# Performance work log

Measured on AMD Instinct MI355X. Metric: run time of the kernel, lower is better.

Reference implementation:

```python
import jax, jax.numpy as jnp
import numpy as np

D = 1024       # d_model
H = 16         # n_heads
N = 8          # ortho_dim
NSKEW = N * (N - 1) // 2
MAX_ANGLE = 0.5
B, T = 4, 4096
IDX_I, IDX_J = np.triu_indices(N, k=1)


def setup_inputs() -> dict:
    key = jax.random.key(0)
    ks = jax.random.split(key, 8)
    s = 0.02
    w = lambda k, shape: jax.random.normal(k, shape, jnp.float32) * s
    return {
        "x": jax.random.normal(ks[0], (B, T, D), jnp.float32),
        "W_skew": w(ks[1], (D, H * NSKEW)),
        "W_k": w(ks[2], (D, H * N)),
        "W_v": w(ks[3], (D, H * N)),
        "W_q": w(ks[4], (D, H * N)),
        "W_beta": w(ks[5], (D, H)),
        "b_beta": w(ks[6], (H,)),
        "W_o": w(ks[7], (H * N, D)),
    }


def _forward(x, W_skew, W_k, W_v, W_q, W_beta, b_beta, W_o):
    Bb, Tt, _ = x.shape
    # skew-symmetric generator -> rotation O_t = expm(skew)
    skew_flat = MAX_ANGLE * jnp.tanh(x @ W_skew).reshape(Bb, Tt, H, NSKEW)
    skew = jnp.zeros((Bb, Tt, H, N, N), x.dtype)
    skew = skew.at[..., IDX_I, IDX_J].set(skew_flat)
    skew = skew.at[..., IDX_J, IDX_I].set(-skew_flat)
    O = jax.vmap(jax.scipy.linalg.expm)(skew.reshape(-1, N, N)).reshape(Bb, Tt, H, N, N)

    k = (x @ W_k).reshape(Bb, Tt, H, N)
    k = k / jnp.maximum(jnp.linalg.norm(k, axis=-1, keepdims=True), 1e-6)
    v = (x @ W_v).reshape(Bb, Tt, H, N)
    q = (x @ W_q).reshape(Bb, Tt, H, N)
    beta = jax.nn.sigmoid(x @ W_beta + b_beta)  # [B,T,H]

    def step(c, inp):
        O_t, k_t, v_t, b_t, q_t = inp  # [B,H,n,n], [B,H,n], ...
        # rotation conjugation: O c O^T
        c_rot = jnp.einsum('bhij,bhjk,bhlk->bhil', O_t, c, O_t)
        # rank-1 erase: c_rot - beta * k (k^T c_rot); rank-1 write: + beta * k v^T
        kc = jnp.einsum('bhi,bhij->bhj', k_t, c_rot)
        b = b_t[..., None, None]
        c_new = c_rot - b * k_t[..., None] * kc[..., None, :] + b * k_t[..., None] * v_t[..., None, :]
        o_t = jnp.einsum('bhi,bhij->bhj', q_t, c_new)  # readout q . c_t
        return c_new, o_t

    c0 = jnp.zeros((Bb, H, N, N), x.dtype)
    tfirst = lambda a: jnp.moveaxis(a, 1, 0)
    _, o = jax.lax.scan(step, c0, (tfirst(O), tfirst(k), tfirst(v), tfirst(beta), tfirst(q)))
    o = jnp.moveaxis(o, 0, 1).reshape(Bb, Tt, H * N)
    return o @ W_o


def reference(x, W_skew, W_k, W_v, W_q, W_beta, b_beta, W_o):
    return _forward(x, W_skew, W_k, W_v, W_q, W_beta, b_beta, W_o)
```

## Files before the change

### kernel.cpp

```cpp
#include <hip/hip_runtime.h>

typedef unsigned short u16;
typedef unsigned int u32;
typedef __attribute__((ext_vector_type(4))) float f32x4;
typedef __attribute__((ext_vector_type(8))) short short8;
typedef __attribute__((ext_vector_type(4))) unsigned int u32x4;

#define DEV __device__ __forceinline__

DEV float bf2f(u16 u){ union{u32 i; float f;} x; x.i = ((u32)u)<<16; return x.f; }
DEV u16 f2bf(float f){ union{u32 i; float f;} x; x.f = f; u32 r = x.i + 0x7fffu + ((x.i>>16)&1u); return (u16)(r>>16); }

union U8 { u16 u[8]; short8 s; };

DEV void gl16(const u16* g, u16* l){
  __builtin_amdgcn_global_load_lds(
      (const __attribute__((address_space(1))) u32*)g,
      (__attribute__((address_space(3))) u32*)l, 16, 0, 0);
}

DEV float fast_htanh(float v){
  float vc = fminf(fmaxf(v, -15.f), 15.f);
  float e = __expf(2.f*vc);
  return 0.5f*(e - 1.f)*__builtin_amdgcn_rcpf(e + 1.f);
}
DEV float fast_sigmoid(float v){
  float e = __expf(-v);
  return __builtin_amdgcn_rcpf(1.f + e);
}

__global__ __launch_bounds__(256) void concat_kernel(
    const float* __restrict__ Wskew, const float* __restrict__ Wk, const float* __restrict__ Wv,
    const float* __restrict__ Wq, const float* __restrict__ Wbeta, const float* __restrict__ Wo,
    u16* __restrict__ Wh, u16* __restrict__ Wl, u16* __restrict__ WoT)
{
  int idx = blockIdx.x*256 + threadIdx.x;
  if (idx < 896*1024){
    int n = idx >> 10, kk = idx & 1023;
    float v;
    if (n < 448)      v = Wskew[kk*448 + n];
    else if (n < 576) v = Wk[kk*128 + (n-448)];
    else if (n < 704) v = Wv[kk*128 + (n-576)];
    else if (n < 832) v = Wq[kk*128 + (n-704)];
    else if (n < 848) v = Wbeta[kk*16 + (n-832)];
    else              v = 0.f;
    u16 h = f2bf(v);
    Wh[idx] = h;
    Wl[idx] = f2bf(v - bf2f(h));
  } else {
    int r = idx - 896*1024;
    int n = r >> 7, kk = r & 127;
    WoT[r] = f2bf(Wo[kk*1024 + n]);
  }
}

__global__ __launch_bounds__(256) void gemm_proj_kernel(
    const float* __restrict__ X,
    const u16* __restrict__ Bh, const u16* __restrict__ Bl,
    float* __restrict__ C, const float* __restrict__ bias)
{
  __shared__ u16 L[2*4*4096];
  const int tid = threadIdx.x;
  const int wave = tid >> 6;
  const int lane = tid & 63;
  const int quad = lane >> 4, l15 = lane & 15;
  const int m0 = blockIdx.x * 128, n0 = blockIdx.y * 128;
  const bool full = (blockIdx.y < 4);
  const int wm = (wave >> 1) * 64, wn = (wave & 1) * 64;
  const bool wantLow = full && !(blockIdx.y == 3 && wn == 64);
  const bool skipBl1 = (blockIdx.y == 3);
  const int K = 1024, ldc = 896;
  const int sr = tid >> 2;
  const int sc = tid & 3;
  const int fS = (sr & 3) ^ ((sr >> 2) & 3);
  const int scS = ((sc ^ fS) << 3);
  const size_t gA0 = (size_t)(m0 + sr)*K + scS, gA1 = gA0 + (size_t)64*K;
  const size_t gB0 = (size_t)(n0 + sr)*K + scS, gB1 = gB0 + (size_t)64*K;
  const int d0 = tid*8, d1 = d0 + 2048;
  const int fR = (l15 & 3) ^ ((l15 >> 2) & 3);
  const int rq = ((quad ^ fR) << 3);

  auto LOADA = [&](int kb, f32x4* va){
    va[0] = *(const f32x4*)(X + gA0 + kb);
    va[1] = *(const f32x4*)(X + gA0 + kb + 4);
    va[2] = *(const f32x4*)(X + gA1 + kb);
    va[3] = *(const f32x4*)(X + gA1 + kb + 4);
  };
  auto WRITEA = [&](int buf, const f32x4* va){
    u16* Lb = L + buf*16384;
    U8 h0, h1;
    #pragma unroll
    for (int e=0;e<4;e++){
      h0.u[e]   = f2bf(va[0][e]);
      h0.u[4+e] = f2bf(va[1][e]);
      h1.u[e]   = f2bf(va[2][e]);
      h1.u[4+e] = f2bf(va[3][e]);
    }
    *(short8*)&Lb[d0] = h0.s; *(short8*)&Lb[d1] = h1.s;
    if (full){
      U8 l0, l1;
      #pragma unroll
      for (int e=0;e<4;e++){
        l0.u[e]   = f2bf(va[0][e] - bf2f(h0.u[e]));
        l0.u[4+e] = f2bf(va[1][e] - bf2f(h0.u[4+e]));
        l1.u[e]   = f2bf(va[2][e] - bf2f(h1.u[e]));
        l1.u[4+e] = f2bf(va[3][e] - bf2f(h1.u[4+e]));
      }
      *(short8*)&Lb[8192+d0] = l0.s; *(short8*)&Lb[8192+d1] = l1.s;
    }
  };
  auto STAGEB = [&](int buf, int kb){
    u16* Lb = L + buf*16384;
    gl16(Bh + gB0 + kb, Lb + 4096 + d0);
    gl16(Bh + gB1 + kb, Lb + 4096 + d1);
    if (full){
      gl16(Bl + gB0 + kb, Lb + 12288 + d0);
      if (!skipBl1) gl16(Bl + gB1 + kb, Lb + 12288 + d1);
    }
  };

  f32x4 acc[4][4] = {};
  { f32x4 va[4]; LOADA(0, va); STAGEB(0, 0); WRITEA(0, va); }
  __syncthreads();
  int cur = 0;
  for (int kb = 0; kb < K; kb += 32){
    const bool hasNext = (kb + 32 < K);
    f32x4 vn[4];
    if (hasNext){ LOADA(kb + 32, vn); STAGEB(cur^1, kb + 32); }
    u16* Lb = L + cur*16384;
    short8 afh[4], bfh[4];
    #pragma unroll
    for (int mi=0;mi<4;mi++) afh[mi] = *(const short8*)&Lb[(wm + mi*16 + l15)*32 + rq];
    #pragma unroll
    for (int ni=0;ni<4;ni++) bfh[ni] = *(const short8*)&Lb[4096 + (wn + ni*16 + l15)*32 + rq];
    #pragma unroll
    for (int mi=0;mi<4;mi++)
      #pragma unroll
      for (int ni=0;ni<4;ni++)
        acc[mi][ni] = __builtin_amdgcn_mfma_f32_16x16x32_bf16(afh[mi], bfh[ni], acc[mi][ni], 0,0,0);
    if (wantLow){
      short8 afl[4], bfl[4];
      #pragma unroll
      for (int mi=0;mi<4;mi++) afl[mi] = *(const short8*)&Lb[8192 + (wm + mi*16 + l15)*32 + rq];
      #pragma unroll
      for (int ni=0;ni<4;ni++) bfl[ni] = *(const short8*)&Lb[12288 + (wn + ni*16 + l15)*32 + rq];
      #pragma unroll
      for (int mi=0;mi<4;mi++)
        #pragma unroll
        for (int ni=0;ni<4;ni++){
          acc[mi][ni] = __builtin_amdgcn_mfma_f32_16x16x32_bf16(afh[mi], bfl[ni], acc[mi][ni], 0,0,0);
          acc[mi][ni] = __builtin_amdgcn_mfma_f32_16x16x32_bf16(afl[mi], bfh[ni], acc[mi][ni], 0,0,0);
        }
    }
    if (hasNext) WRITEA(cur^1, vn);
    __syncthreads();
    cur ^= 1;
  }
  #pragma unroll
  for (int mi=0;mi<4;mi++){
    #pragma unroll
    for (int ni=0;ni<4;ni++){
      const int col = n0 + wn + ni*16 + l15;
      const int rb_ = m0 + wm + mi*16 + quad*4;
      #pragma unroll
      for (int r=0;r<4;r++){
        float v = acc[mi][ni][r];
        const int row = rb_ + r;
        if (col < 448) v = fast_htanh(v);
        else if (col >= 832 && col < 848) v = fast_sigmoid(v + bias[col-832]);
        C[(size_t)row*ldc + col] = v;
      }
    }
  }
}

__global__ __launch_bounds__(256) void gemm_out_kernel(
    const u16* __restrict__ A, const u16* __restrict__ Bt, float* __restrict__ C)
{
  __shared__ u16 L[2*2*4096];
  const int tid = threadIdx.x;
  const int wave = tid >> 6;
  const int lane = tid & 63;
  const int quad = lane >> 4, l15 = lane & 15;
  const int m0 = blockIdx.x * 128, n0 = blockIdx.y * 128;
  const int wm = (wave >> 1) * 64, wn = (wave & 1) * 64;
  const int K = 128, ldc = 1024;
  const int sr = tid >> 2;
  const int sc = tid & 3;
  const int fS = (sr & 3) ^ ((sr >> 2) & 3);
  const int scS = ((sc ^ fS) << 3);
  const size_t gA0 = (size_t)(m0 + sr)*K + scS, gA1 = gA0 + (size_t)64*K;
  const size_t gB0 = (size_t)(n0 + sr)*K + scS, gB1 = gB0 + (size_t)64*K;
  const int d0 = tid*8, d1 = d0 + 2048;
  const int fR = (l15 & 3) ^ ((l15 >> 2) & 3);
  const int rq = ((quad ^ fR) << 3);

  auto STAGE = [&](int buf, int kb){
    u16* Lb = L + buf*8192;
    gl16(A  + gA0 + kb, Lb + d0);
    gl16(A  + gA1 + kb, Lb + d1);
    gl16(Bt + gB0 + kb, Lb + 4096 + d0);
    gl16(Bt + gB1 + kb, Lb + 4096 + d1);
  };

  f32x4 acc[4][4] = {};
  STAGE(0, 0);
  __syncthreads();
  int cur = 0;
  for (int kb = 0; kb < K; kb += 32){
    if (kb + 32 < K) STAGE(cur^1, kb + 32);
    u16* Lb = L + cur*8192;
    short8 af[4], bf8[4];
    #pragma unroll
    for (int mi=0;mi<4;mi++) af[mi] = *(const short8*)&Lb[(wm + mi*16 + l15)*32 + rq];
    #pragma unroll
    for (int ni=0;ni<4;ni++) bf8[ni] = *(const short8*)&Lb[4096 + (wn + ni*16 + l15)*32 + rq];
    #pragma unroll
    for (int mi=0;mi<4;mi++)
      #pragma unroll
      for (int ni=0;ni<4;ni++)
        acc[mi][ni] = __builtin_amdgcn_mfma_f32_16x16x32_bf16(af[mi], bf8[ni], acc[mi][ni], 0,0,0);
    __syncthreads();
    cur ^= 1;
  }
  #pragma unroll
  for (int mi=0;mi<4;mi++)
    #pragma unroll
    for (int ni=0;ni<4;ni++){
      const int col = n0 + wn + ni*16 + l15;
      const int rb_ = m0 + wm + mi*16 + quad*4;
      #pragma unroll
      for (int r=0;r<4;r++)
        C[(size_t)(rb_ + r)*ldc + col] = acc[mi][ni][r];
    }
}

__device__ constexpr int TRI_I[28] = {0,0,0,0,0,0,0, 1,1,1,1,1,1, 2,2,2,2,2, 3,3,3,3, 4,4,4, 5,5, 6};
__device__ constexpr int TRI_J[28] = {1,2,3,4,5,6,7, 2,3,4,5,6,7, 3,4,5,6,7, 4,5,6,7, 5,6,7, 6,7, 7};

__global__ __launch_bounds__(64, 1) void expm_scan_kernel(const float* __restrict__ proj, float* __restrict__ OR)
{
  __shared__ float S0[16*64*4];
  const int t = threadIdx.x;
  const int s = blockIdx.x >> 6, c = blockIdx.x & 63;
  const int b = s >> 4, h = s & 15;
  const int row = b*4096 + c*64 + t;
  const float* sk = proj + (size_t)row*896 + h*28;

  float v[28];
  {
    f32x4 vv[7];
    #pragma unroll
    for (int i=0;i<7;i++) vv[i] = *(const f32x4*)(sk + 4*i);
    #pragma unroll
    for (int i=0;i<28;i++) v[i] = vv[i>>2][i&3] * 0.0625f;
  }

  float M[64], T[64];
  auto bmul = [&](const float* Min, float* Tout){
    #pragma unroll
    for (int i=0;i<8;i++){
      #pragma unroll
      for (int cc=0;cc<8;cc++){
        float acc = 0.f;
        #pragma unroll
        for (int a=0;a<8;a++){
          if (a == i) continue;
          const int k = (i<a) ? (i*7 - (i*(i-1))/2 + a - i - 1)
                              : (a*7 - (a*(a-1))/2 + i - a - 1);
          if (i<a) acc = fmaf( v[k], Min[a*8+cc], acc);
          else     acc = fmaf(-v[k], Min[a*8+cc], acc);
        }
        Tout[i*8+cc] = acc;
      }
    }
  };
  #pragma unroll
  for (int i=0;i<8;i++){
    #pragma unroll
    for (int jj=0;jj<8;jj++){
      float bv = 0.f;
      if (i < jj){ const int k = i*7 - (i*(i-1))/2 + jj - i - 1; bv =  v[k]; }
      if (i > jj){ const int k = jj*7 - (jj*(jj-1))/2 + i - jj - 1; bv = -v[k]; }
      M[i*8+jj] = bv*(1.f/6.f) + ((i==jj)?1.f:0.f);
    }
  }
  const float coef[5] = {0.2f, 0.25f, 1.f/3.f, 0.5f, 1.f};
  #pragma unroll
  for (int st=0; st<5; st++){
    bmul(M, T);
    #pragma unroll
    for (int i=0;i<8;i++)
      #pragma unroll
      for (int jj=0;jj<8;jj++)
        M[i*8+jj] = T[i*8+jj]*coef[st] + ((i==jj)?1.f:0.f);
  }
  #pragma unroll
  for (int sq=0; sq<4; sq++){
    #pragma unroll
    for (int i=0;i<8;i++)
      #pragma unroll
      for (int cc=0;cc<8;cc++){
        float acc = 0.f;
        #pragma unroll
        for (int a=0;a<8;a++) acc = fmaf(M[i*8+a], M[a*8+cc], acc);
        T[i*8+cc] = acc;
      }
    #pragma unroll
    for (int f=0;f<64;f++) M[f] = T[f];
  }
  #pragma unroll
  for (int j=0;j<16;j++){
    f32x4 w = {M[4*j], M[4*j+1], M[4*j+2], M[4*j+3]};
    *(f32x4*)&S0[(j*64 + t)*4] = w;
  }
  __syncthreads();

  #pragma unroll
  for (int d=0; d<6; d++){
    const int off = 1 << d;
    if (t >= off){
      float Q[64];
      #pragma unroll
      for (int j=0;j<16;j++){
        f32x4 x = *(const f32x4*)&S0[(j*64 + (t-off))*4];
        Q[4*j]=x[0]; Q[4*j+1]=x[1]; Q[4*j+2]=x[2]; Q[4*j+3]=x[3];
      }
      #pragma unroll
      for (int i=0;i<8;i++){
        float r[8];
        #pragma unroll
        for (int cc=0;cc<8;cc++){
          float acc = 0.f;
          #pragma unroll
          for (int a=0;a<8;a++) acc = fmaf(M[i*8+a], Q[a*8+cc], acc);
          r[cc] = acc;
        }
        #pragma unroll
        for (int cc=0;cc<8;cc++) M[i*8+cc] = r[cc];
      }
    }
    if (d < 5){
      #pragma unroll
      for (int j=0;j<16;j++){
        f32x4 w = {M[4*j], M[4*j+1], M[4*j+2], M[4*j+3]};
        *(f32x4*)&S0[(j*64 + t)*4] = w;
      }
      __syncthreads();
    }
  }

  float* dst = OR + ((size_t)s*4096 + (size_t)c*64 + t)*64;
  #pragma unroll
  for (int j=0;j<16;j++){
    const int rb = 4*(j&1), col = j>>1;
    f32x4 w = {M[(rb+0)*8 + col], M[(rb+1)*8 + col], M[(rb+2)*8 + col], M[(rb+3)*8 + col]};
    *(f32x4*)(dst + 4*j) = w;
  }
}

DEV void load16(const float* p, f32x4* M){
  #pragma unroll
  for (int q=0;q<16;q++) M[q] = *(const f32x4*)(p + 4*q);
}
DEV void rm_matvec8(const f32x4* M16, const float* x, float* res){
  #pragma unroll
  for (int i=0;i<8;i++){
    float acc = 0.f;
    #pragma unroll
    for (int a=0;a<8;a++) acc = fmaf(M16[2*i + (a>>2)][a&3], x[a], acc);
    res[i] = acc;
  }
}
DEV void cm_matvec8(const f32x4* M16, const float* x, float* res){
  #pragma unroll
  for (int i=0;i<8;i++){
    float acc = 0.f;
    #pragma unroll
    for (int a=0;a<8;a++) acc = fmaf(M16[2*a + (i>>2)][i&3], x[a], acc);
    res[i] = acc;
  }
}

__global__ __launch_bounds__(64, 1) void chunkscan_kernel(const float* __restrict__ OR, float* __restrict__ Rbase)
{
  __shared__ float S[64*68];
  const int t = threadIdx.x;
  const int s = blockIdx.x;
  float M[64];
  const float* qs = OR + ((size_t)s*4096 + (size_t)t*64 + 63)*64;
  #pragma unroll
  for (int j=0;j<16;j++){
    f32x4 x = *(const f32x4*)(qs + 4*j);
    M[4*j]=x[0]; M[4*j+1]=x[1]; M[4*j+2]=x[2]; M[4*j+3]=x[3];
  }
  #pragma unroll
  for (int j=0;j<16;j++){
    f32x4 w = {M[4*j],M[4*j+1],M[4*j+2],M[4*j+3]};
    *(f32x4*)&S[t*68 + 4*j] = w;
  }
  __syncthreads();
  #pragma unroll
  for (int d=0; d<6; d++){
    const int off = 1 << d;
    if (t >= off){
      float Q[64];
      const float* p = &S[(t-off)*68];
      #pragma unroll
      for (int j=0;j<16;j++){
        f32x4 x = *(const f32x4*)(p + 4*j);
        Q[4*j]=x[0]; Q[4*j+1]=x[1]; Q[4*j+2]=x[2]; Q[4*j+3]=x[3];
      }
      float R[64];
      #pragma unroll
      for (int cc=0;cc<8;cc++)
        #pragma unroll
        for (int i=0;i<8;i++){
          float acc = 0.f;
          #pragma unroll
          for (int a=0;a<8;a++) acc = fmaf(M[a*8+i], Q[cc*8+a], acc);
          R[cc*8+i] = acc;
        }
      #pragma unroll
      for (int f=0;f<64;f++) M[f] = R[f];
    }
    if (d < 5){
      #pragma unroll
      for (int j=0;j<16;j++){
        f32x4 w = {M[4*j],M[4*j+1],M[4*j+2],M[4*j+3]};
        *(f32x4*)&S[t*68 + 4*j] = w;
      }
      __syncthreads();
    }
  }
  if (t < 63){
    float* dst = Rbase + ((size_t)s*64 + t + 1)*64;
    #pragma unroll
    for (int j=0;j<16;j++){
      f32x4 w = {M[4*j],M[4*j+1],M[4*j+2],M[4*j+3]};
      *(f32x4*)(dst + 4*j) = w;
    }
  }
  if (t == 0){
    float* dst = Rbase + (size_t)s*64*64;
    #pragma unroll
    for (int cc=0;cc<8;cc++)
      #pragma unroll
      for (int i=0;i<8;i++) dst[cc*8+i] = (i==cc) ? 1.f : 0.f;
  }
}

__global__ __launch_bounds__(256) void rotate_kvq_kernel(const float* __restrict__ OR, const float* __restrict__ Rbase,
    float* __restrict__ proj)
{
  int tid = blockIdx.x*256 + threadIdx.x;
  int s = tid >> 12, t = tid & 4095;
  int c = t >> 6;
  int b = s >> 4, h = s & 15;
  int row = b*4096 + t;
  const float* slot = OR + ((size_t)s*4096 + t)*64;
  float* pr = proj + (size_t)row*896;
  float k[8], v[8], q[8];
  { f32x4 a = *(const f32x4*)(pr+448+h*8), b2 = *(const f32x4*)(pr+452+h*8);
    #pragma unroll
    for (int i=0;i<4;i++){ k[i]=a[i]; k[4+i]=b2[i]; } }
  { f32x4 a = *(const f32x4*)(pr+576+h*8), b2 = *(const f32x4*)(pr+580+h*8);
    #pragma unroll
    for (int i=0;i<4;i++){ v[i]=a[i]; v[4+i]=b2[i]; } }
  { f32x4 a = *(const f32x4*)(pr+704+h*8), b2 = *(const f32x4*)(pr+708+h*8);
    #pragma unroll
    for (int i=0;i<4;i++){ q[i]=a[i]; q[4+i]=b2[i]; } }
  float nn = 0.f;
  #pragma unroll
  for (int i=0;i<8;i++) nn = fmaf(k[i],k[i],nn);
  float inv = 1.f / fmaxf(sqrtf(nn), 1e-6f);
  #pragma unroll
  for (int i=0;i<8;i++) k[i] *= inv;

  f32x4 M[16];
  load16(slot, M);
  float uk[8], uv[8], uq[8];
  rm_matvec8(M, k, uk);
  rm_matvec8(M, v, uv);
  rm_matvec8(M, q, uq);
  load16(Rbase + ((size_t)s*64 + c)*64, M);
  float kt[8], vt[8], qt[8];
  rm_matvec8(M, uk, kt);
  rm_matvec8(M, uv, vt);
  rm_matvec8(M, uq, qt);

  float beta = pr[832+h];
  float qk = 0.f;
  #pragma unroll
  for (int j=0;j<8;j++) qk = fmaf(kt[j], qt[j], qk);
  float* sip = pr + h*28;
  f32x4 w0={kt[0],kt[1],kt[2],kt[3]}, w1={kt[4],kt[5],kt[6],kt[7]};
  f32x4 w2={vt[0],vt[1],vt[2],vt[3]}, w3={vt[4],vt[5],vt[6],vt[7]};
  f32x4 w4={qt[0],qt[1],qt[2],qt[3]}, w5={qt[4],qt[5],qt[6],qt[7]};
  f32x4 w6={beta, qk, 0.f, 0.f};
  *(f32x4*)(sip)=w0; *(f32x4*)(sip+4)=w1; *(f32x4*)(sip+8)=w2; *(f32x4*)(sip+12)=w3;
  *(f32x4*)(sip+16)=w4; *(f32x4*)(sip+20)=w5; *(f32x4*)(sip+24)=w6;
}

__global__ __launch_bounds__(256) void scan_pass1_kernel(const float* __restrict__ proj,
    float* __restrict__ Mbuf, float* __restrict__ wbuf)
{
  int tid = blockIdx.x*256 + threadIdx.x;
  int task = tid >> 3, j = tid & 7;
  int s = task >> 8, c = task & 255;
  int b = s >> 4, h = s & 15;
  const float* rec = proj + ((size_t)b*4096 + (size_t)c*16)*896 + h*28;
  float m[8], w[8];
  #pragma unroll
  for (int i=0;i<8;i++){ m[i] = (i==j)?1.f:0.f; w[i] = 0.f; }
  f32x4 k0 = *(const f32x4*)(rec), k1 = *(const f32x4*)(rec+4);
  float vt = rec[8+j];
  float beta = rec[24];
  for (int tt=0; tt<16; tt++){
    const float* pn = rec + (size_t)(tt+1)*896;
    f32x4 nk0 = *(const f32x4*)(pn), nk1 = *(const f32x4*)(pn+4);
    float nvt = pn[8+j];
    float nbeta = pn[24];
    float s1, s2;
    s1 = ((k0[0]*m[0] + k0[1]*m[1]) + (k0[2]*m[2] + k0[3]*m[3]))
       + ((k1[0]*m[4] + k1[1]*m[5]) + (k1[2]*m[6] + k1[3]*m[7]));
    s2 = ((k0[0]*w[0] + k0[1]*w[1]) + (k0[2]*w[2] + k0[3]*w[3]))
       + ((k1[0]*w[4] + k1[1]*w[5]) + (k1[2]*w[6] + k1[3]*w[7]));
    float c1 = -beta*s1, c2 = beta*(vt - s2);
    #pragma unroll
    for (int i=0;i<4;i++){ m[i] = fmaf(k0[i], c1, m[i]); m[4+i] = fmaf(k1[i], c1, m[4+i]); }
    #pragma unroll
    for (int i=0;i<4;i++){ w[i] = fmaf(k0[i], c2, w[i]); w[4+i] = fmaf(k1[i], c2, w[4+i]); }
    k0=nk0; k1=nk1; vt=nvt; beta=nbeta;
  }
  float* md = Mbuf + (size_t)task*64 + j*8;
  float* wd = wbuf + (size_t)task*64 + j*8;
  f32x4 m0={m[0],m[1],m[2],m[3]}, m1={m[4],m[5],m[6],m[7]};
  f32x4 w0={w[0],w[1],w[2],w[3]}, w1={w[4],w[5],w[6],w[7]};
  *(f32x4*)(md) = m0; *(f32x4*)(md+4) = m1;
  *(f32x4*)(wd) = w0; *(f32x4*)(wd+4) = w1;
}

__global__ __launch_bounds__(512) void scan_mid_kernel(const float* __restrict__ Mbuf,
    const float* __restrict__ wbuf, float* __restrict__ dstart)
{
  __shared__ float SM[256*68];
  __shared__ float SW[256*68];
  const int tid = threadIdx.x;
  const int c = tid >> 1, g = tid & 1;
  const int s = blockIdx.x;
  const size_t base = (size_t)s*256*64;
  const float* mp = Mbuf + base + (size_t)c*64 + 32*g;
  const float* wp = wbuf + base + (size_t)c*64 + 32*g;
  float W[32];
  {
    float* sm = &SM[c*68 + 32*g];
    float* sw = &SW[c*68 + 32*g];
    #pragma unroll
    for (int j=0;j<8;j++){
      f32x4 a = *(const f32x4*)(mp + 4*j);
      f32x4 b = *(const f32x4*)(wp + 4*j);
      *(f32x4*)(sm + 4*j) = a;
      *(f32x4*)(sw + 4*j) = b;
      W[4*j]=b[0]; W[4*j+1]=b[1]; W[4*j+2]=b[2]; W[4*j+3]=b[3];
    }
  }
  __syncthreads();
  for (int d=0; d<8; d++){
    const int off = 1 << d;
    const bool act = (c >= off);
    float Mo[64], pM[32], pW[32];
    if (act){
      const float* om = &SM[c*68];
      #pragma unroll
      for (int j=0;j<16;j++){
        f32x4 x = *(const f32x4*)(om + 4*j);
        Mo[4*j]=x[0]; Mo[4*j+1]=x[1]; Mo[4*j+2]=x[2]; Mo[4*j+3]=x[3];
      }
      const float* qm = &SM[(c-off)*68 + 32*g];
      const float* qw = &SW[(c-off)*68 + 32*g];
      #pragma unroll
      for (int j=0;j<8;j++){
        f32x4 x = *(const f32x4*)(qm + 4*j);
        f32x4 y = *(const f32x4*)(qw + 4*j);
        pM[4*j]=x[0]; pM[4*j+1]=x[1]; pM[4*j+2]=x[2]; pM[4*j+3]=x[3];
        pW[4*j]=y[0]; pW[4*j+1]=y[1]; pW[4*j+2]=y[2]; pW[4*j+3]=y[3];
      }
    }
    __syncthreads();
    if (act){
      float nM[32], nW[32];
      #pragma unroll
      for (int cl=0; cl<4; cl++){
        #pragma unroll
        for (int i=0;i<8;i++){
          float aM = 0.f, aW = 0.f;
          #pragma unroll
          for (int a=0;a<8;a++){
            aM = fmaf(Mo[a*8+i], pM[cl*8+a], aM);
            aW = fmaf(Mo[a*8+i], pW[cl*8+a], aW);
          }
          nM[cl*8+i] = aM;
          nW[cl*8+i] = aW + W[cl*8+i];
        }
      }
      float* sm = &SM[c*68 + 32*g];
      float* sw = &SW[c*68 + 32*g];
      #pragma unroll
      for (int j=0;j<8;j++){
        f32x4 x = {nM[4*j], nM[4*j+1], nM[4*j+2], nM[4*j+3]};
        f32x4 y = {nW[4*j], nW[4*j+1], nW[4*j+2], nW[4*j+3]};
        *(f32x4*)(sm + 4*j) = x;
        *(f32x4*)(sw + 4*j) = y;
      }
      #pragma unroll
      for (int f=0;f<32;f++) W[f] = nW[f];
    }
    __syncthreads();
  }
  if (c < 255){
    float* dd = dstart + base + (size_t)(c+1)*64 + 32*g;
    #pragma unroll
    for (int j=0;j<8;j++){
      f32x4 y = {W[4*j],W[4*j+1],W[4*j+2],W[4*j+3]};
      *(f32x4*)(dd + 4*j) = y;
    }
  }
  if (c == 0){
    float* dd = dstart + base + 32*g;
    f32x4 z = {0.f,0.f,0.f,0.f};
    #pragma unroll
    for (int j=0;j<8;j++) *(f32x4*)(dd + 4*j) = z;
  }
}

__global__ __launch_bounds__(256) void scan_pass2_kernel(const float* __restrict__ proj,
    const float* __restrict__ dstart, float* __restrict__ oo)
{
  int tid = blockIdx.x*256 + threadIdx.x;
  int task = tid >> 3, j = tid & 7;
  int s = task >> 8, c = task & 255;
  int b = s >> 4, h = s & 15;
  const float* rec = proj + ((size_t)b*4096 + (size_t)c*16)*896 + h*28;
  float* op = oo + (((size_t)s*4096 + (size_t)c*16)*8) + j;
  float d[8];
  { const float* ds = dstart + (size_t)task*64 + j*8;
    f32x4 a = *(const f32x4*)(ds), b2 = *(const f32x4*)(ds+4);
    #pragma unroll
    for (int i=0;i<4;i++){ d[i]=a[i]; d[4+i]=b2[i]; } }
  f32x4 k0 = *(const f32x4*)(rec),    k1 = *(const f32x4*)(rec+4);
  f32x4 q0 = *(const f32x4*)(rec+16), q1 = *(const f32x4*)(rec+20);
  f32x4 mb = *(const f32x4*)(rec+24);
  float vt = rec[8+j];
  for (int tt=0; tt<16; tt++){
    const float* pn = rec + (size_t)(tt+1)*896;
    f32x4 nk0 = *(const f32x4*)(pn),    nk1 = *(const f32x4*)(pn+4);
    f32x4 nq0 = *(const f32x4*)(pn+16), nq1 = *(const f32x4*)(pn+20);
    f32x4 nmb = *(const f32x4*)(pn+24);
    float nvt = pn[8+j];
    float kd, qd;
    kd = ((k0[0]*d[0] + k0[1]*d[1]) + (k0[2]*d[2] + k0[3]*d[3]))
       + ((k1[0]*d[4] + k1[1]*d[5]) + (k1[2]*d[6] + k1[3]*d[7]));
    qd = ((q0[0]*d[0] + q0[1]*d[1]) + (q0[2]*d[2] + q0[3]*d[3]))
       + ((q1[0]*d[4] + q1[1]*d[5]) + (q1[2]*d[6] + q1[3]*d[7]));
    float w_ = mb[0] * (vt - kd);
    #pragma unroll
    for (int i=0;i<4;i++){ d[i] = fmaf(k0[i], w_, d[i]); d[4+i] = fmaf(k1[i], w_, d[4+i]); }
    op[(size_t)tt*8] = fmaf(mb[1], w_, qd);
    k0=nk0; k1=nk1; q0=nq0; q1=nq1; mb=nmb; vt=nvt;
  }
}

__global__ __launch_bounds__(256) void rotout_kernel(const float* __restrict__ OR, const float* __restrict__ Rbase,
                                                     const float* __restrict__ oo, u16* __restrict__ obf)
{
  int tid = blockIdx.x*256 + threadIdx.x;
  int s = tid >> 12, t = tid & 4095;
  int c = t >> 6;
  int b = s >> 4, h = s & 15;
  int row = b*4096 + t;
  float u[8];
  { const float* up = oo + ((size_t)s*4096 + t)*8;
    f32x4 a = *(const f32x4*)(up), b2 = *(const f32x4*)(up+4);
    #pragma unroll
    for (int i=0;i<4;i++){ u[i]=a[i]; u[4+i]=b2[i]; } }
  f32x4 M[16];
  load16(Rbase + ((size_t)s*64 + c)*64, M);
  float w[8];
  cm_matvec8(M, u, w);
  load16(OR + ((size_t)s*4096 + t)*64, M);
  float o[8];
  cm_matvec8(M, w, o);
  u32 p0 = (u32)f2bf(o[0]) | ((u32)f2bf(o[1])<<16);
  u32 p1 = (u32)f2bf(o[2]) | ((u32)f2bf(o[3])<<16);
  u32 p2 = (u32)f2bf(o[4]) | ((u32)f2bf(o[5])<<16);
  u32 p3 = (u32)f2bf(o[6]) | ((u32)f2bf(o[7])<<16);
  u32x4 pk = {p0,p1,p2,p3};
  *(u32x4*)(void*)(obf + (size_t)row*128 + h*8) = pk;
}

extern "C" void kernel_launch(void* const* d_in, const int* in_sizes, int n_in,
                              void* d_out, int out_size, void* d_ws, size_t ws_size,
                              hipStream_t stream)
{
  const float* x     = (const float*)d_in[0];
  const float* Wskew = (const float*)d_in[1];
  const float* Wk    = (const float*)d_in[2];
  const float* Wv    = (const float*)d_in[3];
  const float* Wq    = (const float*)d_in[4];
  const float* Wbeta = (const float*)d_in[5];
  const float* bbeta = (const float*)d_in[6];
  const float* Wo    = (const float*)d_in[7];

  char* w = (char*)d_ws; size_t off = 0;
  auto alloc = [&](size_t bytes)->void*{ void* p = w + off; off += (bytes + 255) & ~(size_t)255; return p; };
  u16*   Wh     = (u16*)  alloc((size_t)896*1024*2);
  u16*   Wl     = (u16*)  alloc((size_t)896*1024*2);
  u16*   WoT    = (u16*)  alloc((size_t)1024*128*2);
  float* proj   = (float*)alloc((size_t)16384*896*4);
  float* OR     = (float*)alloc((size_t)262144*64*4);
  float* Rbase  = (float*)alloc((size_t)64*64*64*4);
  float* oo     = (float*)alloc((size_t)262144*8*4);
  float* Mbuf   = (float*)alloc((size_t)16384*64*4);
  float* wbuf   = (float*)alloc((size_t)16384*64*4);
  float* dstart = (float*)alloc((size_t)16384*64*4);
  u16*   obf    = (u16*)proj;

  hipLaunchKernelGGL(concat_kernel, dim3(4096), dim3(256), 0, stream,
                     Wskew, Wk, Wv, Wq, Wbeta, Wo, Wh, Wl, WoT);
  hipLaunchKernelGGL(gemm_proj_kernel, dim3(128,7), dim3(256), 0, stream,
                     x, Wh, Wl, proj, bbeta);
  hipLaunchKernelGGL(expm_scan_kernel, dim3(4096), dim3(64), 0, stream, proj, OR);
  hipLaunchKernelGGL(chunkscan_kernel, dim3(64), dim3(64), 0, stream, OR, Rbase);
  hipLaunchKernelGGL(rotate_kvq_kernel, dim3(1024), dim3(256), 0, stream, OR, Rbase, proj);
  hipLaunchKernelGGL(scan_pass1_kernel, dim3(512), dim3(256), 0, stream, proj, Mbuf, wbuf);
  hipLaunchKernelGGL(scan_mid_kernel, dim3(64), dim3(512), 0, stream, Mbuf, wbuf, dstart);
  hipLaunchKernelGGL(scan_pass2_kernel, dim3(512), dim3(256), 0, stream, proj, dstart, oo);
  hipLaunchKernelGGL(rotout_kernel, dim3(1024), dim3(256), 0, stream, OR, Rbase, oo, obf);
  hipLaunchKernelGGL(gemm_out_kernel, dim3(128,8), dim3(256), 0, stream,
                     obf, WoT, (float*)d_out);
}
```

Before: 363.8 us.

## Pre-split x to bf16 hi/lo and fuse local k/v/q rotation into expm kernel

A new kernel converts x once into bf16 high and low parts, so the projection GEMM can stage A tiles with direct global-to-LDS loads instead of loading fp32 and converting in registers on every block column. The expm/scan kernel now also normalizes k and applies its in-chunk rotation to k, v and q while M is still in registers. That removes the reread of the per-token 64-float OR matrices in rotate_kvq, which now only applies the chunk base rotation. The cost is an extra pass that writes 64 MB of split x into the OR buffer, plus more register pressure and work in the expm kernel.

```diff
diff --git a/kernel.cpp b/kernel.cpp
--- a/kernel.cpp
+++ b/kernel.cpp
@@ -27,6 +27,21 @@
 DEV float fast_sigmoid(float v){
   float e = __expf(-v);
   return __builtin_amdgcn_rcpf(1.f + e);
+}
+
+__global__ __launch_bounds__(256) void splitx_kernel(const float* __restrict__ x,
+    u16* __restrict__ xh, u16* __restrict__ xl)
+{
+  size_t base = ((size_t)blockIdx.x*256 + threadIdx.x) * 8;
+  f32x4 a = *(const f32x4*)(x + base), b = *(const f32x4*)(x + base + 4);
+  U8 h, l;
+  #pragma unroll
+  for (int e=0;e<4;e++){
+    u16 hh = f2bf(a[e]); h.u[e]   = hh; l.u[e]   = f2bf(a[e] - bf2f(hh));
+    u16 gg = f2bf(b[e]); h.u[4+e] = gg; l.u[4+e] = f2bf(b[e] - bf2f(gg));
+  }
+  *(short8*)(xh + base) = h.s;
+  *(short8*)(xl + base) = l.s;
 }
 
 __global__ __launch_bounds__(256) void concat_kernel(
@@ -55,7 +70,7 @@
 }
 
 __global__ __launch_bounds__(256) void gemm_proj_kernel(
-    const float* __restrict__ X,
+    const u16* __restrict__ Ah, const u16* __restrict__ Al,
     const u16* __restrict__ Bh, const u16* __restrict__ Bl,
     float* __restrict__ C, const float* __restrict__ bias)
 {
@@ -80,53 +95,26 @@
   const int fR = (l15 & 3) ^ ((l15 >> 2) & 3);
   const int rq = ((quad ^ fR) << 3);
 
-  auto LOADA = [&](int kb, f32x4* va){
-    va[0] = *(const f32x4*)(X + gA0 + kb);
-    va[1] = *(const f32x4*)(X + gA0 + kb + 4);
-    va[2] = *(const f32x4*)(X + gA1 + kb);
-    va[3] = *(const f32x4*)(X + gA1 + kb + 4);
-  };
-  auto WRITEA = [&](int buf, const f32x4* va){
+  auto STAGE = [&](int buf, int kb){
     u16* Lb = L + buf*16384;
-    U8 h0, h1;
-    #pragma unroll
-    for (int e=0;e<4;e++){
-      h0.u[e]   = f2bf(va[0][e]);
-      h0.u[4+e] = f2bf(va[1][e]);
-      h1.u[e]   = f2bf(va[2][e]);
-      h1.u[4+e] = f2bf(va[3][e]);
-    }
-    *(short8*)&Lb[d0] = h0.s; *(short8*)&Lb[d1] = h1.s;
-    if (full){
-      U8 l0, l1;
-      #pragma unroll
-      for (int e=0;e<4;e++){
-        l0.u[e]   = f2bf(va[0][e] - bf2f(h0.u[e]));
-        l0.u[4+e] = f2bf(va[1][e] - bf2f(h0.u[4+e]));
-        l1.u[e]   = f2bf(va[2][e] - bf2f(h1.u[e]));
-        l1.u[4+e] = f2bf(va[3][e] - bf2f(h1.u[4+e]));
-      }
-      *(short8*)&Lb[8192+d0] = l0.s; *(short8*)&Lb[8192+d1] = l1.s;
-    }
-  };
-  auto STAGEB = [&](int buf, int kb){
-    u16* Lb = L + buf*16384;
+    gl16(Ah + gA0 + kb, Lb + d0);
+    gl16(Ah + gA1 + kb, Lb + d1);
     gl16(Bh + gB0 + kb, Lb + 4096 + d0);
     gl16(Bh + gB1 + kb, Lb + 4096 + d1);
     if (full){
+      gl16(Al + gA0 + kb, Lb + 8192 + d0);
+      gl16(Al + gA1 + kb, Lb + 8192 + d1);
       gl16(Bl + gB0 + kb, Lb + 12288 + d0);
       if (!skipBl1) gl16(Bl + gB1 + kb, Lb + 12288 + d1);
     }
   };
 
   f32x4 acc[4][4] = {};
-  { f32x4 va[4]; LOADA(0, va); STAGEB(0, 0); WRITEA(0, va); }
+  STAGE(0, 0);
   __syncthreads();
   int cur = 0;
   for (int kb = 0; kb < K; kb += 32){
-    const bool hasNext = (kb + 32 < K);
-    f32x4 vn[4];
-    if (hasNext){ LOADA(kb + 32, vn); STAGEB(cur^1, kb + 32); }
+    if (kb + 32 < K) STAGE(cur^1, kb + 32);
     u16* Lb = L + cur*16384;
     short8 afh[4], bfh[4];
     #pragma unroll
@@ -152,7 +140,6 @@
           acc[mi][ni] = __builtin_amdgcn_mfma_f32_16x16x32_bf16(afl[mi], bfh[ni], acc[mi][ni], 0,0,0);
         }
     }
-    if (hasNext) WRITEA(cur^1, vn);
     __syncthreads();
     cur ^= 1;
   }
@@ -238,14 +225,15 @@
 __device__ constexpr int TRI_I[28] = {0,0,0,0,0,0,0, 1,1,1,1,1,1, 2,2,2,2,2, 3,3,3,3, 4,4,4, 5,5, 6};
 __device__ constexpr int TRI_J[28] = {1,2,3,4,5,6,7, 2,3,4,5,6,7, 3,4,5,6,7, 4,5,6,7, 5,6,7, 6,7, 7};
 
-__global__ __launch_bounds__(64, 1) void expm_scan_kernel(const float* __restrict__ proj, float* __restrict__ OR)
+__global__ __launch_bounds__(64, 1) void expm_scan_kernel(float* __restrict__ proj, float* __restrict__ OR)
 {
   __shared__ float S0[16*64*4];
   const int t = threadIdx.x;
   const int s = blockIdx.x >> 6, c = blockIdx.x & 63;
   const int b = s >> 4, h = s & 15;
   const int row = b*4096 + c*64 + t;
-  const float* sk = proj + (size_t)row*896 + h*28;
+  float* pr = proj + (size_t)row*896;
+  const float* sk = pr + h*28;
 
   float v[28];
   {
@@ -357,6 +345,45 @@
     f32x4 w = {M[(rb+0)*8 + col], M[(rb+1)*8 + col], M[(rb+2)*8 + col], M[(rb+3)*8 + col]};
     *(f32x4*)(dst + 4*j) = w;
   }
+
+  float kk[8], vv2[8], qq[8];
+  { f32x4 a = *(const f32x4*)(pr+448+h*8), b2 = *(const f32x4*)(pr+452+h*8);
+    #pragma unroll
+    for (int i=0;i<4;i++){ kk[i]=a[i]; kk[4+i]=b2[i]; } }
+  { f32x4 a = *(const f32x4*)(pr+576+h*8), b2 = *(const f32x4*)(pr+580+h*8);
+    #pragma unroll
+    for (int i=0;i<4;i++){ vv2[i]=a[i]; vv2[4+i]=b2[i]; } }
+  { f32x4 a = *(const f32x4*)(pr+704+h*8), b2 = *(const f32x4*)(pr+708+h*8);
+    #pragma unroll
+    for (int i=0;i<4;i++){ qq[i]=a[i]; qq[4+i]=b2[i]; } }
+  float nn = 0.f;
+  #pragma unroll
+  for (int i=0;i<8;i++) nn = fmaf(kk[i],kk[i],nn);
+  float inv = 1.f / fmaxf(sqrtf(nn), 1e-6f);
+  #pragma unroll
+  for (int i=0;i<8;i++) kk[i] *= inv;
+  float uk[8], uv[8], uq[8];
+  #pragma unroll
+  for (int a=0;a<8;a++){
+    float sk_=0.f, sv_=0.f, sq_=0.f;
+    #pragma unroll
+    for (int i=0;i<8;i++){
+      float m = M[i*8+a];
+      sk_ = fmaf(m, kk[i], sk_); sv_ = fmaf(m, vv2[i], sv_); sq_ = fmaf(m, qq[i], sq_);
+    }
+    uk[a]=sk_; uv[a]=sv_; uq[a]=sq_;
+  }
+  float beta = pr[832+h];
+  float qk = 0.f;
+  #pragma unroll
+  for (int a=0;a<8;a++) qk = fmaf(uk[a], uq[a], qk);
+  float* sip = pr + h*28;
+  f32x4 w0={uk[0],uk[1],uk[2],uk[3]}, w1={uk[4],uk[5],uk[6],uk[7]};
+  f32x4 w2={uv[0],uv[1],uv[2],uv[3]}, w3={uv[4],uv[5],uv[6],uv[7]};
+  f32x4 w4={uq[0],uq[1],uq[2],uq[3]}, w5={uq[4],uq[5],uq[6],uq[7]};
+  f32x4 w6={beta, qk, 0.f, 0.f};
+  *(f32x4*)(sip)=w0; *(f32x4*)(sip+4)=w1; *(f32x4*)(sip+8)=w2; *(f32x4*)(sip+12)=w3;
+  *(f32x4*)(sip+16)=w4; *(f32x4*)(sip+20)=w5; *(f32x4*)(sip+24)=w6;
 }
 
 DEV void load16(const float* p, f32x4* M){
@@ -450,7 +477,7 @@
   }
 }
 
-__global__ __launch_bounds__(256) void rotate_kvq_kernel(const float* __restrict__ OR, const float* __restrict__ Rbase,
+__global__ __launch_bounds__(256) void rotate_kvq_kernel(const float* __restrict__ Rbase,
     float* __restrict__ proj)
 {
   int tid = blockIdx.x*256 + threadIdx.x;
@@ -458,48 +485,28 @@
   int c = t >> 6;
   int b = s >> 4, h = s & 15;
   int row = b*4096 + t;
-  const float* slot = OR + ((size_t)s*4096 + t)*64;
-  float* pr = proj + (size_t)row*896;
-  float k[8], v[8], q[8];
-  { f32x4 a = *(const f32x4*)(pr+448+h*8), b2 = *(const f32x4*)(pr+452+h*8);
-    #pragma unroll
-    for (int i=0;i<4;i++){ k[i]=a[i]; k[4+i]=b2[i]; } }
-  { f32x4 a = *(const f32x4*)(pr+576+h*8), b2 = *(const f32x4*)(pr+580+h*8);
-    #pragma unroll
-    for (int i=0;i<4;i++){ v[i]=a[i]; v[4+i]=b2[i]; } }
-  { f32x4 a = *(const f32x4*)(pr+704+h*8), b2 = *(const f32x4*)(pr+708+h*8);
-    #pragma unroll
-    for (int i=0;i<4;i++){ q[i]=a[i]; q[4+i]=b2[i]; } }
-  float nn = 0.f;
-  #pragma unroll
-  for (int i=0;i<8;i++) nn = fmaf(k[i],k[i],nn);
-  float inv = 1.f / fmaxf(sqrtf(nn), 1e-6f);
-  #pragma unroll
-  for (int i=0;i<8;i++) k[i] *= inv;
-
+  float* sip = proj + (size_t)row*896 + h*28;
+  float uk[8], uv[8], uq[8];
+  { f32x4 a = *(const f32x4*)(sip),    b2 = *(const f32x4*)(sip+4);
+    #pragma unroll
+    for (int i=0;i<4;i++){ uk[i]=a[i]; uk[4+i]=b2[i]; } }
+  { f32x4 a = *(const f32x4*)(sip+8),  b2 = *(const f32x4*)(sip+12);
+    #pragma unroll
+    for (int i=0;i<4;i++){ uv[i]=a[i]; uv[4+i]=b2[i]; } }
+  { f32x4 a = *(const f32x4*)(sip+16), b2 = *(const f32x4*)(sip+20);
+    #pragma unroll
+    for (int i=0;i<4;i++){ uq[i]=a[i]; uq[4+i]=b2[i]; } }
   f32x4 M[16];
-  load16(slot, M);
-  float uk[8], uv[8], uq[8];
-  rm_matvec8(M, k, uk);
-  rm_matvec8(M, v, uv);
-  rm_matvec8(M, q, uq);
   load16(Rbase + ((size_t)s*64 + c)*64, M);
   float kt[8], vt[8], qt[8];
   rm_matvec8(M, uk, kt);
   rm_matvec8(M, uv, vt);
   rm_matvec8(M, uq, qt);
-
-  float beta = pr[832+h];
-  float qk = 0.f;
-  #pragma unroll
-  for (int j=0;j<8;j++) qk = fmaf(kt[j], qt[j], qk);
-  float* sip = pr + h*28;
   f32x4 w0={kt[0],kt[1],kt[2],kt[3]}, w1={kt[4],kt[5],kt[6],kt[7]};
   f32x4 w2={vt[0],vt[1],vt[2],vt[3]}, w3={vt[4],vt[5],vt[6],vt[7]};
   f32x4 w4={qt[0],qt[1],qt[2],qt[3]}, w5={qt[4],qt[5],qt[6],qt[7]};
-  f32x4 w6={beta, qk, 0.f, 0.f};
   *(f32x4*)(sip)=w0; *(f32x4*)(sip+4)=w1; *(f32x4*)(sip+8)=w2; *(f32x4*)(sip+12)=w3;
-  *(f32x4*)(sip+16)=w4; *(f32x4*)(sip+20)=w5; *(f32x4*)(sip+24)=w6;
+  *(f32x4*)(sip+16)=w4; *(f32x4*)(sip+20)=w5;
 }
 
 __global__ __launch_bounds__(256) void scan_pass1_kernel(const float* __restrict__ proj,
@@ -724,15 +731,18 @@
   float* Mbuf   = (float*)alloc((size_t)16384*64*4);
   float* wbuf   = (float*)alloc((size_t)16384*64*4);
   float* dstart = (float*)alloc((size_t)16384*64*4);
+  u16*   xh     = (u16*)OR;
+  u16*   xl     = xh + (size_t)16384*1024;
   u16*   obf    = (u16*)proj;
 
+  hipLaunchKernelGGL(splitx_kernel, dim3(8192), dim3(256), 0, stream, x, xh, xl);
   hipLaunchKernelGGL(concat_kernel, dim3(4096), dim3(256), 0, stream,
                      Wskew, Wk, Wv, Wq, Wbeta, Wo, Wh, Wl, WoT);
   hipLaunchKernelGGL(gemm_proj_kernel, dim3(128,7), dim3(256), 0, stream,
-                     x, Wh, Wl, proj, bbeta);
+                     xh, xl, Wh, Wl, proj, bbeta);
   hipLaunchKernelGGL(expm_scan_kernel, dim3(4096), dim3(64), 0, stream, proj, OR);
   hipLaunchKernelGGL(chunkscan_kernel, dim3(64), dim3(64), 0, stream, OR, Rbase);
-  hipLaunchKernelGGL(rotate_kvq_kernel, dim3(1024), dim3(256), 0, stream, OR, Rbase, proj);
+  hipLaunchKernelGGL(rotate_kvq_kernel, dim3(1024), dim3(256), 0, stream, Rbase, proj);
   hipLaunchKernelGGL(scan_pass1_kernel, dim3(512), dim3(256), 0, stream, proj, Mbuf, wbuf);
   hipLaunchKernelGGL(scan_mid_kernel, dim3(64), dim3(512), 0, stream, Mbuf, wbuf, dstart);
   hipLaunchKernelGGL(scan_pass2_kernel, dim3(512), dim3(256), 0, stream, proj, dstart, oo);
```

After: 374.2 us. 2.9% more time.
